# Kernel tuning notes

Measured on AMD Instinct MI355X. Metric: run time of the kernel, lower is better.

## Reference

```python
import jax, jax.numpy as jnp
import numpy as np

H = 1024
V = 50257
S = 2048


def setup_inputs() -> dict:
    key = jax.random.key(0)
    ks = jax.random.split(key, 16)
    sc = 0.05
    return {
        "input_ids": jax.random.randint(ks[0], (1,), 0, V, dtype=jnp.int64)
        if jax.config.jax_enable_x64
        else jax.random.randint(ks[0], (1,), 0, V, dtype=jnp.int32),
        "h0": jax.random.normal(ks[1], (1, 1, H), dtype=jnp.float32),
        "c0": jax.random.normal(ks[2], (1, 1, H), dtype=jnp.float32),
        "encoder_hiddens": jax.random.normal(ks[3], (1, S, H), dtype=jnp.float32),
        "embedding": jax.random.normal(ks[4], (V, H), dtype=jnp.float32) * sc,
        "attn_W": jax.random.normal(ks[5], (1, 2 * H), dtype=jnp.float32) * sc,
        "attn_b": jax.random.normal(ks[6], (1,), dtype=jnp.float32) * sc,
        "comb_W": jax.random.normal(ks[7], (H, 2 * H), dtype=jnp.float32) * sc,
        "comb_b": jax.random.normal(ks[8], (H,), dtype=jnp.float32) * sc,
        "W_ih": jax.random.normal(ks[9], (4 * H, H), dtype=jnp.float32) * sc,
        "W_hh": jax.random.normal(ks[10], (4 * H, H), dtype=jnp.float32) * sc,
        "b_ih": jax.random.normal(ks[11], (4 * H,), dtype=jnp.float32) * sc,
        "b_hh": jax.random.normal(ks[12], (4 * H,), dtype=jnp.float32) * sc,
        "out_W": jax.random.normal(ks[13], (V, H), dtype=jnp.float32) * sc,
        "out_b": jax.random.normal(ks[14], (V,), dtype=jnp.float32) * sc,
    }


def reference(input_ids, h0, c0, encoder_hiddens, embedding, attn_W, attn_b,
              comb_W, comb_b, W_ih, W_hh, b_ih, b_hh, out_W, out_b):
    x = embedding[input_ids[0]]          # [H] embedded token
    h = h0[0, 0]                          # [H]
    c = c0[0, 0]                          # [H]
    enc = encoder_hiddens[0]              # [S, H]

    # attention: linear score per position (NO softmax in original), then
    # context = enc^T @ coeff
    hiddens = jnp.concatenate([enc, jnp.broadcast_to(h, enc.shape)], axis=1)  # [S, 2H]
    coeff = hiddens @ attn_W.T + attn_b   # [S, 1]
    context = (enc.T @ coeff)[:, 0]       # [H]

    combined = jnp.concatenate([x, context]) @ comb_W.T + comb_b  # [H]
    z = jax.nn.relu(combined)

    # single LSTM step, PyTorch gate order i, f, g, o
    gates = W_ih @ z + b_ih + W_hh @ h + b_hh  # [4H]
    i, f, g, o = jnp.split(gates, 4)
    i = jax.nn.sigmoid(i)
    f = jax.nn.sigmoid(f)
    g = jnp.tanh(g)
    o = jax.nn.sigmoid(o)
    c_new = f * c + i * g
    h_new = o * jnp.tanh(c_new)

    logits = h_new @ out_W.T + out_b      # [V]
    logp = jax.nn.log_softmax(logits)[None, :]  # [1, V]
    return logp, h_new[None, None, :], c_new[None, None, :]
```

## Files before the change

kernel.cpp:

```cpp
#include <hip/hip_runtime.h>
#include <math.h>

#define H 1024
#define V 50257
#define S 2048
#define NCH 128
#define NPART 3142

#define O_CTXP   0
#define O_CTX    131072
#define O_Z      132096
#define O_GPRE   133120
#define O_HNEW   137216
#define O_PART   138240

__device__ inline float wred_sum(float v) {
    for (int o = 32; o > 0; o >>= 1) v += __shfl_down(v, o, 64);
    return v;
}
__device__ inline float sigm(float x) { return 1.f / (1.f + expf(-x)); }
__device__ inline float dot4(float4 a, float4 b) {
    return a.x*b.x + a.y*b.y + a.z*b.z + a.w*b.w;
}

__global__ __launch_bounds__(256) void k_attn(const float* __restrict__ enc,
        const float* __restrict__ h0, const float* __restrict__ attn_W,
        const float* __restrict__ attn_b, const float* __restrict__ W_hh,
        const float* __restrict__ b_ih, const float* __restrict__ b_hh,
        float* __restrict__ ws) {
    const int b = blockIdx.x, t = threadIdx.x, lane = t & 63, wave = t >> 6;
    if (b < NCH) {
        __shared__ float sred[4];
        __shared__ float scoef[16];
        float4 hv4 = ((const float4*)h0)[t];
        float4 wv4 = ((const float4*)(attn_W + H))[t];
        float p = wred_sum(dot4(hv4, wv4));
        if (lane == 0) sred[wave] = p;
        __syncthreads();
        const float hdot = sred[0] + sred[1] + sred[2] + sred[3] + attn_b[0];
        const float4* w0 = (const float4*)attn_W;
        const int s0 = b * 16;
        {
            int sb = s0 + wave * 4;
            const float4* e0 = (const float4*)(enc + (size_t)(sb    ) * H);
            const float4* e1 = (const float4*)(enc + (size_t)(sb + 1) * H);
            const float4* e2 = (const float4*)(enc + (size_t)(sb + 2) * H);
            const float4* e3 = (const float4*)(enc + (size_t)(sb + 3) * H);
            float a0 = 0.f, a1 = 0.f, a2 = 0.f, a3 = 0.f;
            #pragma unroll
            for (int kk = 0; kk < 4; ++kk) {
                int k4 = kk * 64 + lane;
                float4 w = w0[k4];
                a0 += dot4(e0[k4], w); a1 += dot4(e1[k4], w);
                a2 += dot4(e2[k4], w); a3 += dot4(e3[k4], w);
            }
            a0 = wred_sum(a0); a1 = wred_sum(a1);
            a2 = wred_sum(a2); a3 = wred_sum(a3);
            if (lane == 0) {
                scoef[wave*4 + 0] = a0 + hdot;
                scoef[wave*4 + 1] = a1 + hdot;
                scoef[wave*4 + 2] = a2 + hdot;
                scoef[wave*4 + 3] = a3 + hdot;
            }
        }
        __syncthreads();
        float4 a4 = make_float4(0.f, 0.f, 0.f, 0.f);
        #pragma unroll 4
        for (int rr = 0; rr < 16; ++rr) {
            float c = scoef[rr];
            float4 e = ((const float4*)(enc + (size_t)(s0 + rr) * H))[t];
            a4.x += c * e.x; a4.y += c * e.y; a4.z += c * e.z; a4.w += c * e.w;
        }
        ((float4*)(ws + O_CTXP + b * H))[t] = a4;
    } else {
        const int bb = b - NCH;
        float4 hr[4];
        #pragma unroll
        for (int kk = 0; kk < 4; ++kk) hr[kk] = ((const float4*)h0)[kk*64 + lane];
        const int r0 = bb * 16 + wave * 4;
        const float4* m0 = (const float4*)(W_hh + (size_t)(r0    ) * H);
        const float4* m1 = (const float4*)(W_hh + (size_t)(r0 + 1) * H);
        const float4* m2 = (const float4*)(W_hh + (size_t)(r0 + 2) * H);
        const float4* m3 = (const float4*)(W_hh + (size_t)(r0 + 3) * H);
        float a0 = 0.f, a1 = 0.f, a2 = 0.f, a3 = 0.f;
        #pragma unroll
        for (int kk = 0; kk < 4; ++kk) {
            int k4 = kk * 64 + lane;
            float4 a = hr[kk];
            a0 += dot4(m0[k4], a); a1 += dot4(m1[k4], a);
            a2 += dot4(m2[k4], a); a3 += dot4(m3[k4], a);
        }
        a0 = wred_sum(a0); a1 = wred_sum(a1);
        a2 = wred_sum(a2); a3 = wred_sum(a3);
        if (lane == 0) {
            ws[O_GPRE + r0    ] = a0 + b_ih[r0    ] + b_hh[r0    ];
            ws[O_GPRE + r0 + 1] = a1 + b_ih[r0 + 1] + b_hh[r0 + 1];
            ws[O_GPRE + r0 + 2] = a2 + b_ih[r0 + 2] + b_hh[r0 + 2];
            ws[O_GPRE + r0 + 3] = a3 + b_ih[r0 + 3] + b_hh[r0 + 3];
        }
    }
}

__global__ __launch_bounds__(256) void k_ctx(float* __restrict__ ws) {
    const int b = blockIdx.x, t = threadIdx.x;
    const int jj = t & 15, cg = t >> 4;
    const int j0 = b * 16;
    float acc = 0.f;
    #pragma unroll
    for (int k = 0; k < 8; ++k)
        acc += ws[O_CTXP + (size_t)(cg + 16*k) * H + j0 + jj];
    __shared__ float sarr[256];
    sarr[t] = acc;
    __syncthreads();
    if (t < 16) {
        float a = 0.f;
        #pragma unroll
        for (int g = 0; g < 16; ++g) a += sarr[g * 16 + t];
        ws[O_CTX + j0 + t] = a;
    }
}

__global__ __launch_bounds__(256) void k_z(const float* __restrict__ emb,
        const int* __restrict__ ids, const float* __restrict__ comb_W,
        const float* __restrict__ comb_b, float* __restrict__ ws) {
    const int b = blockIdx.x, t = threadIdx.x, lane = t & 63, wave = t >> 6;
    const int tok = ids[0];
    const int i = b * 4 + wave;
    const float4* wrow = (const float4*)(comb_W + (size_t)i * 2 * H);
    const float4* x4 = (const float4*)(emb + (size_t)tok * H);
    const float4* c4 = (const float4*)(ws + O_CTX);
    float acc = 0.f;
    #pragma unroll
    for (int kk = 0; kk < 4; ++kk) {
        int k4 = kk * 64 + lane;
        acc += dot4(wrow[k4], x4[k4]);
        acc += dot4(wrow[256 + k4], c4[k4]);
    }
    acc = wred_sum(acc);
    if (lane == 0) ws[O_Z + i] = fmaxf(acc + comb_b[i], 0.f);
}

__global__ __launch_bounds__(256) void k_gates_lstm(const float* __restrict__ W_ih,
        const float* __restrict__ c0, float* __restrict__ ws, float* __restrict__ out) {
    const int j = blockIdx.x, t = threadIdx.x, lane = t & 63, g = t >> 6;
    __shared__ float sg[4];
    const int row = g * H + j;
    const float4* wi = (const float4*)(W_ih + (size_t)row * H);
    const float4* zv = (const float4*)(ws + O_Z);
    float acc = 0.f;
    #pragma unroll
    for (int kk = 0; kk < 4; ++kk) {
        int k4 = kk * 64 + lane;
        acc += dot4(wi[k4], zv[k4]);
    }
    acc = wred_sum(acc);
    if (lane == 0) sg[g] = acc + ws[O_GPRE + row];
    __syncthreads();
    if (t == 0) {
        float ig = sigm(sg[0]);
        float fg = sigm(sg[1]);
        float gg = tanhf(sg[2]);
        float og = sigm(sg[3]);
        float cn = fg * c0[j] + ig * gg;
        float hn = og * tanhf(cn);
        out[V + j]     = hn;
        out[V + H + j] = cn;
        ws[O_HNEW + j] = hn;
    }
}

__global__ __launch_bounds__(256) void k_logits(const float* __restrict__ out_W,
        const float* __restrict__ out_b, float* __restrict__ ws,
        float* __restrict__ out) {
    const int t = threadIdx.x, lane = t & 63, wave = t >> 6;
    __shared__ float slg[16];
    const float4* hv = (const float4*)(ws + O_HNEW);
    float4 hr[4];
    #pragma unroll
    for (int kk = 0; kk < 4; ++kk) hr[kk] = hv[kk * 64 + lane];
    const int v0 = blockIdx.x * 16 + wave * 4;
    const bool q0 = v0 < V, q1 = v0 + 1 < V, q2 = v0 + 2 < V, q3 = v0 + 3 < V;
    const float4* w0 = (const float4*)(out_W + (size_t)(q0 ? v0     : 0) * H);
    const float4* w1 = (const float4*)(out_W + (size_t)(q1 ? v0 + 1 : 0) * H);
    const float4* w2 = (const float4*)(out_W + (size_t)(q2 ? v0 + 2 : 0) * H);
    const float4* w3 = (const float4*)(out_W + (size_t)(q3 ? v0 + 3 : 0) * H);
    float a0 = 0.f, a1 = 0.f, a2 = 0.f, a3 = 0.f;
    #pragma unroll
    for (int kk = 0; kk < 4; ++kk) {
        int k4 = kk * 64 + lane;
        float4 a = hr[kk];
        a0 += dot4(w0[k4], a); a1 += dot4(w1[k4], a);
        a2 += dot4(w2[k4], a); a3 += dot4(w3[k4], a);
    }
    a0 = wred_sum(a0); a1 = wred_sum(a1);
    a2 = wred_sum(a2); a3 = wred_sum(a3);
    if (lane == 0) {
        float l0 = a0 + out_b[q0 ? v0     : 0];
        float l1 = a1 + out_b[q1 ? v0 + 1 : 0];
        float l2 = a2 + out_b[q2 ? v0 + 2 : 0];
        float l3 = a3 + out_b[q3 ? v0 + 3 : 0];
        if (q0) out[v0    ] = l0;
        if (q1) out[v0 + 1] = l1;
        if (q2) out[v0 + 2] = l2;
        if (q3) out[v0 + 3] = l3;
        slg[wave*4 + 0] = q0 ? l0 : -1e30f;
        slg[wave*4 + 1] = q1 ? l1 : -1e30f;
        slg[wave*4 + 2] = q2 ? l2 : -1e30f;
        slg[wave*4 + 3] = q3 ? l3 : -1e30f;
    }
    __syncthreads();
    if (t == 0) {
        float m = slg[0];
        #pragma unroll
        for (int i = 1; i < 16; ++i) m = fmaxf(m, slg[i]);
        float s = 0.f;
        #pragma unroll
        for (int i = 0; i < 16; ++i) s += expf(slg[i] - m);
        ws[O_PART + 2 * blockIdx.x]     = m;
        ws[O_PART + 2 * blockIdx.x + 1] = s;
    }
}

__global__ __launch_bounds__(1024) void k_logp(const float* __restrict__ ws,
        float* __restrict__ out) {
    const int t = threadIdx.x, lane = t & 63, wv = t >> 6;
    __shared__ float smm[16], sss[16];
    __shared__ float slse;
    float m = -1e30f, s = 0.f;
    for (int i = t; i < NPART; i += 1024) {
        float m2 = ws[O_PART + 2 * i], s2 = ws[O_PART + 2 * i + 1];
        float M = fmaxf(m, m2);
        s = s * expf(m - M) + s2 * expf(m2 - M);
        m = M;
    }
    for (int o = 32; o > 0; o >>= 1) {
        float m2 = __shfl_down(m, o, 64), s2 = __shfl_down(s, o, 64);
        float M = fmaxf(m, m2);
        s = s * expf(m - M) + s2 * expf(m2 - M);
        m = M;
    }
    if (lane == 0) { smm[wv] = m; sss[wv] = s; }
    __syncthreads();
    if (t == 0) {
        float M = smm[0], Ssum = sss[0];
        #pragma unroll
        for (int i = 1; i < 16; ++i) {
            float MM = fmaxf(M, smm[i]);
            Ssum = Ssum * expf(M - MM) + sss[i] * expf(smm[i] - MM);
            M = MM;
        }
        slse = M + logf(Ssum);
    }
    __syncthreads();
    const float lse = slse;
    const int v = blockIdx.x * 1024 + t;
    if (v < V) out[v] = out[v] - lse;
}

extern "C" void kernel_launch(void* const* d_in, const int* in_sizes, int n_in,
                              void* d_out, int out_size, void* d_ws, size_t ws_size,
                              hipStream_t stream) {
    const int*   ids    = (const int*)  d_in[0];
    const float* h0     = (const float*)d_in[1];
    const float* c0     = (const float*)d_in[2];
    const float* enc    = (const float*)d_in[3];
    const float* emb    = (const float*)d_in[4];
    const float* attn_W = (const float*)d_in[5];
    const float* attn_b = (const float*)d_in[6];
    const float* comb_W = (const float*)d_in[7];
    const float* comb_b = (const float*)d_in[8];
    const float* W_ih   = (const float*)d_in[9];
    const float* W_hh   = (const float*)d_in[10];
    const float* b_ih   = (const float*)d_in[11];
    const float* b_hh   = (const float*)d_in[12];
    const float* out_W  = (const float*)d_in[13];
    const float* out_b  = (const float*)d_in[14];
    float* out = (float*)d_out;
    float* ws  = (float*)d_ws;

    k_attn      <<<NCH + 256, 256, 0, stream>>>(enc, h0, attn_W, attn_b,
                                                W_hh, b_ih, b_hh, ws);
    k_ctx       <<<64, 256, 0, stream>>>(ws);
    k_z         <<<256, 256, 0, stream>>>(emb, ids, comb_W, comb_b, ws);
    k_gates_lstm<<<1024, 256, 0, stream>>>(W_ih, c0, ws, out);
    k_logits    <<<NPART, 256, 0, stream>>>(out_W, out_b, ws, out);
    k_logp      <<<64, 1024, 0, stream>>>(ws, out);
}
```

Before: 71.58 us.

## Fold context reduction into k_z, coarsen attention chunks and logits blocks

The attention kernel now processes 64 encoder rows per block (32 chunks instead of 128), so the partial-context buffer shrinks. The separate k_ctx reduction kernel is removed: each k_z block sums the 32 partial contexts into shared memory before its matvec, saving one launch at the cost of redundant reduction work in every block. The logits kernel uses 512 threads and 32 rows per block, halving the partial count that k_logp must combine. The attention stage now runs fewer blocks, each doing more serial work.

```diff
diff --git a/kernel.cpp b/kernel.cpp
--- a/kernel.cpp
+++ b/kernel.cpp
@@ -4,15 +4,15 @@
 #define H 1024
 #define V 50257
 #define S 2048
-#define NCH 128
-#define NPART 3142
+#define NCH 32
+#define LROWS 32
+#define NPART 1571
 
 #define O_CTXP   0
-#define O_CTX    131072
-#define O_Z      132096
-#define O_GPRE   133120
-#define O_HNEW   137216
-#define O_PART   138240
+#define O_Z      32768
+#define O_GPRE   33792
+#define O_HNEW   37888
+#define O_PART   38912
 
 __device__ inline float wred_sum(float v) {
     for (int o = 32; o > 0; o >>= 1) v += __shfl_down(v, o, 64);
@@ -31,7 +31,7 @@
     const int b = blockIdx.x, t = threadIdx.x, lane = t & 63, wave = t >> 6;
     if (b < NCH) {
         __shared__ float sred[4];
-        __shared__ float scoef[16];
+        __shared__ float scoef[64];
         float4 hv4 = ((const float4*)h0)[t];
         float4 wv4 = ((const float4*)(attn_W + H))[t];
         float p = wred_sum(dot4(hv4, wv4));
@@ -39,9 +39,10 @@
         __syncthreads();
         const float hdot = sred[0] + sred[1] + sred[2] + sred[3] + attn_b[0];
         const float4* w0 = (const float4*)attn_W;
-        const int s0 = b * 16;
-        {
-            int sb = s0 + wave * 4;
+        const int s0 = b * 64;
+        #pragma unroll
+        for (int gq = 0; gq < 4; ++gq) {
+            int sb = s0 + wave * 16 + gq * 4;
             const float4* e0 = (const float4*)(enc + (size_t)(sb    ) * H);
             const float4* e1 = (const float4*)(enc + (size_t)(sb + 1) * H);
             const float4* e2 = (const float4*)(enc + (size_t)(sb + 2) * H);
@@ -57,16 +58,16 @@
             a0 = wred_sum(a0); a1 = wred_sum(a1);
             a2 = wred_sum(a2); a3 = wred_sum(a3);
             if (lane == 0) {
-                scoef[wave*4 + 0] = a0 + hdot;
-                scoef[wave*4 + 1] = a1 + hdot;
-                scoef[wave*4 + 2] = a2 + hdot;
-                scoef[wave*4 + 3] = a3 + hdot;
+                scoef[wave*16 + gq*4 + 0] = a0 + hdot;
+                scoef[wave*16 + gq*4 + 1] = a1 + hdot;
+                scoef[wave*16 + gq*4 + 2] = a2 + hdot;
+                scoef[wave*16 + gq*4 + 3] = a3 + hdot;
             }
         }
         __syncthreads();
         float4 a4 = make_float4(0.f, 0.f, 0.f, 0.f);
-        #pragma unroll 4
-        for (int rr = 0; rr < 16; ++rr) {
+        #pragma unroll 8
+        for (int rr = 0; rr < 64; ++rr) {
             float c = scoef[rr];
             float4 e = ((const float4*)(enc + (size_t)(s0 + rr) * H))[t];
             a4.x += c * e.x; a4.y += c * e.y; a4.z += c * e.z; a4.w += c * e.w;
@@ -101,34 +102,25 @@
     }
 }
 
-__global__ __launch_bounds__(256) void k_ctx(float* __restrict__ ws) {
-    const int b = blockIdx.x, t = threadIdx.x;
-    const int jj = t & 15, cg = t >> 4;
-    const int j0 = b * 16;
-    float acc = 0.f;
-    #pragma unroll
-    for (int k = 0; k < 8; ++k)
-        acc += ws[O_CTXP + (size_t)(cg + 16*k) * H + j0 + jj];
-    __shared__ float sarr[256];
-    sarr[t] = acc;
-    __syncthreads();
-    if (t < 16) {
-        float a = 0.f;
-        #pragma unroll
-        for (int g = 0; g < 16; ++g) a += sarr[g * 16 + t];
-        ws[O_CTX + j0 + t] = a;
-    }
-}
-
 __global__ __launch_bounds__(256) void k_z(const float* __restrict__ emb,
         const int* __restrict__ ids, const float* __restrict__ comb_W,
         const float* __restrict__ comb_b, float* __restrict__ ws) {
     const int b = blockIdx.x, t = threadIdx.x, lane = t & 63, wave = t >> 6;
+    __shared__ __align__(16) float sctx[H];
+    float4 a4 = make_float4(0.f, 0.f, 0.f, 0.f);
+    #pragma unroll 8
+    for (int ch = 0; ch < NCH; ++ch) {
+        float4 v = ((const float4*)(ws + O_CTXP + ch * H))[t];
+        a4.x += v.x; a4.y += v.y; a4.z += v.z; a4.w += v.w;
+    }
+    ((float4*)sctx)[t] = a4;
+    __syncthreads();
+
     const int tok = ids[0];
     const int i = b * 4 + wave;
     const float4* wrow = (const float4*)(comb_W + (size_t)i * 2 * H);
     const float4* x4 = (const float4*)(emb + (size_t)tok * H);
-    const float4* c4 = (const float4*)(ws + O_CTX);
+    const float4* c4 = (const float4*)sctx;
     float acc = 0.f;
     #pragma unroll
     for (int kk = 0; kk < 4; ++kk) {
@@ -169,16 +161,16 @@
     }
 }
 
-__global__ __launch_bounds__(256) void k_logits(const float* __restrict__ out_W,
+__global__ __launch_bounds__(512) void k_logits(const float* __restrict__ out_W,
         const float* __restrict__ out_b, float* __restrict__ ws,
         float* __restrict__ out) {
     const int t = threadIdx.x, lane = t & 63, wave = t >> 6;
-    __shared__ float slg[16];
+    __shared__ float slg[32];
     const float4* hv = (const float4*)(ws + O_HNEW);
     float4 hr[4];
     #pragma unroll
     for (int kk = 0; kk < 4; ++kk) hr[kk] = hv[kk * 64 + lane];
-    const int v0 = blockIdx.x * 16 + wave * 4;
+    const int v0 = blockIdx.x * LROWS + wave * 4;
     const bool q0 = v0 < V, q1 = v0 + 1 < V, q2 = v0 + 2 < V, q3 = v0 + 3 < V;
     const float4* w0 = (const float4*)(out_W + (size_t)(q0 ? v0     : 0) * H);
     const float4* w1 = (const float4*)(out_W + (size_t)(q1 ? v0 + 1 : 0) * H);
@@ -212,10 +204,10 @@
     if (t == 0) {
         float m = slg[0];
         #pragma unroll
-        for (int i = 1; i < 16; ++i) m = fmaxf(m, slg[i]);
+        for (int i = 1; i < 32; ++i) m = fmaxf(m, slg[i]);
         float s = 0.f;
         #pragma unroll
-        for (int i = 0; i < 16; ++i) s += expf(slg[i] - m);
+        for (int i = 0; i < 32; ++i) s += expf(slg[i] - m);
         ws[O_PART + 2 * blockIdx.x]     = m;
         ws[O_PART + 2 * blockIdx.x + 1] = s;
     }
@@ -280,9 +272,8 @@
 
     k_attn      <<<NCH + 256, 256, 0, stream>>>(enc, h0, attn_W, attn_b,
                                                 W_hh, b_ih, b_hh, ws);
-    k_ctx       <<<64, 256, 0, stream>>>(ws);
     k_z         <<<256, 256, 0, stream>>>(emb, ids, comb_W, comb_b, ws);
     k_gates_lstm<<<1024, 256, 0, stream>>>(W_ih, c0, ws, out);
-    k_logits    <<<NPART, 256, 0, stream>>>(out_W, out_b, ws, out);
+    k_logits    <<<NPART, 512, 0, stream>>>(out_W, out_b, ws, out);
     k_logp      <<<64, 1024, 0, stream>>>(ws, out);
 }
```

Measured after the change: 70.82 us. About the same (-1.1%).

## Fuse context reduction into combine kernel and reshape logits to one row per wave

Applied to the files above, without the earlier changes.

The separate k_ctx launch goes away. Each k_z block now reduces the 128 context partials into shared memory itself, then computes 16 combine rows with 2 rows per wave. Every one of the 64 blocks repeats the same 512KB partial reduction, which adds redundant L2 traffic in exchange for one fewer launch. k_logits changes from 4 rows per wave in 256-thread blocks to 1 row per wave in 512-thread blocks. This doubles the number of partial max/sum pairs that k_logp has to combine, but may expose more memory parallelism per row.

```diff
diff --git a/kernel.cpp b/kernel.cpp
--- a/kernel.cpp
+++ b/kernel.cpp
@@ -5,14 +5,13 @@
 #define V 50257
 #define S 2048
 #define NCH 128
-#define NPART 3142
+#define NLOG 6283
 
 #define O_CTXP   0
-#define O_CTX    131072
-#define O_Z      132096
-#define O_GPRE   133120
-#define O_HNEW   137216
-#define O_PART   138240
+#define O_Z      131072
+#define O_GPRE   132096
+#define O_HNEW   136192
+#define O_PART   137216
 
 __device__ inline float wred_sum(float v) {
     for (int o = 32; o > 0; o >>= 1) v += __shfl_down(v, o, 64);
@@ -101,43 +100,50 @@
     }
 }
 
-__global__ __launch_bounds__(256) void k_ctx(float* __restrict__ ws) {
-    const int b = blockIdx.x, t = threadIdx.x;
-    const int jj = t & 15, cg = t >> 4;
-    const int j0 = b * 16;
-    float acc = 0.f;
-    #pragma unroll
-    for (int k = 0; k < 8; ++k)
-        acc += ws[O_CTXP + (size_t)(cg + 16*k) * H + j0 + jj];
-    __shared__ float sarr[256];
-    sarr[t] = acc;
-    __syncthreads();
-    if (t < 16) {
-        float a = 0.f;
-        #pragma unroll
-        for (int g = 0; g < 16; ++g) a += sarr[g * 16 + t];
-        ws[O_CTX + j0 + t] = a;
-    }
-}
-
-__global__ __launch_bounds__(256) void k_z(const float* __restrict__ emb,
+__global__ __launch_bounds__(512) void k_z(const float* __restrict__ emb,
         const int* __restrict__ ids, const float* __restrict__ comb_W,
         const float* __restrict__ comb_b, float* __restrict__ ws) {
     const int b = blockIdx.x, t = threadIdx.x, lane = t & 63, wave = t >> 6;
+    __shared__ __align__(16) float spart[2][H];
+    __shared__ __align__(16) float sctx[H];
+    {
+        const int half = t >> 8, fi = t & 255;
+        float4 a4 = make_float4(0.f, 0.f, 0.f, 0.f);
+        #pragma unroll 8
+        for (int ch = half * 64; ch < half * 64 + 64; ++ch) {
+            float4 v = ((const float4*)(ws + O_CTXP + ch * H))[fi];
+            a4.x += v.x; a4.y += v.y; a4.z += v.z; a4.w += v.w;
+        }
+        ((float4*)spart[half])[fi] = a4;
+    }
+    __syncthreads();
+    if (t < 256) {
+        float4 p0 = ((const float4*)spart[0])[t];
+        float4 p1 = ((const float4*)spart[1])[t];
+        p0.x += p1.x; p0.y += p1.y; p0.z += p1.z; p0.w += p1.w;
+        ((float4*)sctx)[t] = p0;
+    }
+    __syncthreads();
+
     const int tok = ids[0];
-    const int i = b * 4 + wave;
-    const float4* wrow = (const float4*)(comb_W + (size_t)i * 2 * H);
     const float4* x4 = (const float4*)(emb + (size_t)tok * H);
-    const float4* c4 = (const float4*)(ws + O_CTX);
-    float acc = 0.f;
+    const float4* c4 = (const float4*)sctx;
+    const int i0 = b * 16 + wave * 2;
+    const float4* wr0 = (const float4*)(comb_W + (size_t)i0 * 2 * H);
+    const float4* wr1 = (const float4*)(comb_W + (size_t)(i0 + 1) * 2 * H);
+    float a0 = 0.f, a1 = 0.f;
     #pragma unroll
     for (int kk = 0; kk < 4; ++kk) {
         int k4 = kk * 64 + lane;
-        acc += dot4(wrow[k4], x4[k4]);
-        acc += dot4(wrow[256 + k4], c4[k4]);
-    }
-    acc = wred_sum(acc);
-    if (lane == 0) ws[O_Z + i] = fmaxf(acc + comb_b[i], 0.f);
+        float4 xv = x4[k4], cv = c4[k4];
+        a0 += dot4(wr0[k4], xv) + dot4(wr0[256 + k4], cv);
+        a1 += dot4(wr1[k4], xv) + dot4(wr1[256 + k4], cv);
+    }
+    a0 = wred_sum(a0); a1 = wred_sum(a1);
+    if (lane == 0) {
+        ws[O_Z + i0    ] = fmaxf(a0 + comb_b[i0    ], 0.f);
+        ws[O_Z + i0 + 1] = fmaxf(a1 + comb_b[i0 + 1], 0.f);
+    }
 }
 
 __global__ __launch_bounds__(256) void k_gates_lstm(const float* __restrict__ W_ih,
@@ -169,53 +175,38 @@
     }
 }
 
-__global__ __launch_bounds__(256) void k_logits(const float* __restrict__ out_W,
+__global__ __launch_bounds__(512) void k_logits(const float* __restrict__ out_W,
         const float* __restrict__ out_b, float* __restrict__ ws,
         float* __restrict__ out) {
     const int t = threadIdx.x, lane = t & 63, wave = t >> 6;
-    __shared__ float slg[16];
+    __shared__ float slg[8];
     const float4* hv = (const float4*)(ws + O_HNEW);
     float4 hr[4];
     #pragma unroll
     for (int kk = 0; kk < 4; ++kk) hr[kk] = hv[kk * 64 + lane];
-    const int v0 = blockIdx.x * 16 + wave * 4;
-    const bool q0 = v0 < V, q1 = v0 + 1 < V, q2 = v0 + 2 < V, q3 = v0 + 3 < V;
-    const float4* w0 = (const float4*)(out_W + (size_t)(q0 ? v0     : 0) * H);
-    const float4* w1 = (const float4*)(out_W + (size_t)(q1 ? v0 + 1 : 0) * H);
-    const float4* w2 = (const float4*)(out_W + (size_t)(q2 ? v0 + 2 : 0) * H);
-    const float4* w3 = (const float4*)(out_W + (size_t)(q3 ? v0 + 3 : 0) * H);
-    float a0 = 0.f, a1 = 0.f, a2 = 0.f, a3 = 0.f;
+    const int v = blockIdx.x * 8 + wave;
+    const bool q = v < V;
+    const float4* wr = (const float4*)(out_W + (size_t)(q ? v : 0) * H);
+    float acc = 0.f;
     #pragma unroll
     for (int kk = 0; kk < 4; ++kk) {
         int k4 = kk * 64 + lane;
-        float4 a = hr[kk];
-        a0 += dot4(w0[k4], a); a1 += dot4(w1[k4], a);
-        a2 += dot4(w2[k4], a); a3 += dot4(w3[k4], a);
-    }
-    a0 = wred_sum(a0); a1 = wred_sum(a1);
-    a2 = wred_sum(a2); a3 = wred_sum(a3);
+        acc += dot4(wr[k4], hr[kk]);
+    }
+    acc = wred_sum(acc);
     if (lane == 0) {
-        float l0 = a0 + out_b[q0 ? v0     : 0];
-        float l1 = a1 + out_b[q1 ? v0 + 1 : 0];
-        float l2 = a2 + out_b[q2 ? v0 + 2 : 0];
-        float l3 = a3 + out_b[q3 ? v0 + 3 : 0];
-        if (q0) out[v0    ] = l0;
-        if (q1) out[v0 + 1] = l1;
-        if (q2) out[v0 + 2] = l2;
-        if (q3) out[v0 + 3] = l3;
-        slg[wave*4 + 0] = q0 ? l0 : -1e30f;
-        slg[wave*4 + 1] = q1 ? l1 : -1e30f;
-        slg[wave*4 + 2] = q2 ? l2 : -1e30f;
-        slg[wave*4 + 3] = q3 ? l3 : -1e30f;
+        float lg = acc + out_b[q ? v : 0];
+        if (q) out[v] = lg;
+        slg[wave] = q ? lg : -1e30f;
     }
     __syncthreads();
     if (t == 0) {
         float m = slg[0];
         #pragma unroll
-        for (int i = 1; i < 16; ++i) m = fmaxf(m, slg[i]);
+        for (int i = 1; i < 8; ++i) m = fmaxf(m, slg[i]);
         float s = 0.f;
         #pragma unroll
-        for (int i = 0; i < 16; ++i) s += expf(slg[i] - m);
+        for (int i = 0; i < 8; ++i) s += expf(slg[i] - m);
         ws[O_PART + 2 * blockIdx.x]     = m;
         ws[O_PART + 2 * blockIdx.x + 1] = s;
     }
@@ -227,7 +218,7 @@
     __shared__ float smm[16], sss[16];
     __shared__ float slse;
     float m = -1e30f, s = 0.f;
-    for (int i = t; i < NPART; i += 1024) {
+    for (int i = t; i < NLOG; i += 1024) {
         float m2 = ws[O_PART + 2 * i], s2 = ws[O_PART + 2 * i + 1];
         float M = fmaxf(m, m2);
         s = s * expf(m - M) + s2 * expf(m2 - M);
@@ -280,9 +271,8 @@
 
     k_attn      <<<NCH + 256, 256, 0, stream>>>(enc, h0, attn_W, attn_b,
                                                 W_hh, b_ih, b_hh, ws);
-    k_ctx       <<<64, 256, 0, stream>>>(ws);
-    k_z         <<<256, 256, 0, stream>>>(emb, ids, comb_W, comb_b, ws);
+    k_z         <<<64, 512, 0, stream>>>(emb, ids, comb_W, comb_b, ws);
     k_gates_lstm<<<1024, 256, 0, stream>>>(W_ih, c0, ws, out);
-    k_logits    <<<NPART, 256, 0, stream>>>(out_W, out_b, ws, out);
+    k_logits    <<<NLOG, 512, 0, stream>>>(out_W, out_b, ws, out);
     k_logp      <<<64, 1024, 0, stream>>>(ws, out);
 }
```

After: 63.23 us. -11.7%, faster.
